# Performance work log

Measured on AMD Instinct MI355X. Metric: run time of the kernel, lower is better.

## Reference

```python
import jax, jax.numpy as jnp
import numpy as np

B, N, C = 4, 2048, 768
H = 12
DH = C // H
HID = int(C * 4.0)
SCALE = DH ** -0.5
EPS = 1e-5


def layernorm(x, g, b):
    mu = jnp.mean(x, axis=-1, keepdims=True)
    var = jnp.var(x, axis=-1, keepdims=True)
    return (x - mu) * jax.lax.rsqrt(var + EPS) * g + b


def setup_inputs() -> dict:
    key = jax.random.key(0)
    ks = jax.random.split(key, 10)
    s = lambda fan_in: 1.0 / np.sqrt(fan_in)
    return {
        "x": jax.random.normal(ks[0], (B, N, C), dtype=jnp.float32),
        "ln1_g": jnp.ones((C,), jnp.float32),
        "ln1_b": jnp.zeros((C,), jnp.float32),
        "w_qkv": jax.random.uniform(ks[1], (C, 3 * C), jnp.float32, -s(C), s(C)),
        "w_proj": jax.random.uniform(ks[2], (C, C), jnp.float32, -s(C), s(C)),
        "b_proj": jnp.zeros((C,), jnp.float32),
        "ln2_g": jnp.ones((C,), jnp.float32),
        "ln2_b": jnp.zeros((C,), jnp.float32),
        "w_fc1": jax.random.uniform(ks[3], (C, HID), jnp.float32, -s(C), s(C)),
        "b_fc1": jnp.zeros((HID,), jnp.float32),
        "w_fc2": jax.random.uniform(ks[4], (HID, C), jnp.float32, -s(HID), s(HID)),
        "b_fc2": jnp.zeros((C,), jnp.float32),
    }


def reference(x, ln1_g, ln1_b, w_qkv, w_proj, b_proj, ln2_g, ln2_b, w_fc1, b_fc1, w_fc2, b_fc2):
    # --- attention branch ---
    h = layernorm(x, ln1_g, ln1_b)                       # [B,N,C]
    qkv = (h @ w_qkv).reshape(B, N, 3, H, DH)
    q = qkv[:, :, 0].transpose(0, 2, 1, 3)               # [B,H,N,DH]
    k = qkv[:, :, 1].transpose(0, 2, 1, 3)
    v = qkv[:, :, 2].transpose(0, 2, 1, 3)
    attn = jnp.einsum('bhnd,bhmd->bhnm', q, k) * SCALE   # [B,H,N,N]
    attn = jax.nn.softmax(attn, axis=-1)
    y = jnp.einsum('bhnm,bhmd->bhnd', attn, v)           # [B,H,N,DH]
    y = y.transpose(0, 2, 1, 3).reshape(B, N, C)
    y = y @ w_proj + b_proj
    x = x + y
    # --- MLP branch ---
    h = layernorm(x, ln2_g, ln2_b)
    h = jax.nn.gelu(h @ w_fc1 + b_fc1, approximate=False)
    h = h @ w_fc2 + b_fc2
    return x + h
```

## Files before the change

kernel.cpp:

```cpp
#include <hip/hip_runtime.h>
#include <stdint.h>

#define DEV __device__ __forceinline__

typedef __attribute__((ext_vector_type(8))) short bf16x8;
typedef __attribute__((ext_vector_type(4))) float f32x4;
typedef __attribute__((ext_vector_type(4))) short s16x4;

DEV short f2bf(float f) {
    union { float f; unsigned u; } v; v.f = f;
    unsigned r = v.u + 0x7fffu + ((v.u >> 16) & 1u);
    return (short)(r >> 16);
}

DEV uint32_t cvtpk(float lo, float hi) {
    uint32_t r;
    asm("v_cvt_pk_bf16_f32 %0, %1, %2" : "=v"(r) : "v"(lo), "v"(hi));
    return r;
}

typedef const unsigned int __attribute__((address_space(1)))* gp1;
typedef unsigned int __attribute__((address_space(3)))* lp3;

DEV void gload16(const void* g, void* l) {
    __builtin_amdgcn_global_load_lds((gp1)g, (lp3)l, 16, 0, 0);
}

DEV void wait4_barrier() { asm volatile("s_waitcnt vmcnt(4)\ns_barrier" ::: "memory"); }
DEV void wait2_barrier() { asm volatile("s_waitcnt vmcnt(2)\ns_barrier" ::: "memory"); }
DEV void wait0_barrier() { asm volatile("s_waitcnt vmcnt(0)\ns_barrier" ::: "memory"); }

__global__ __launch_bounds__(256) void tcvt(
    const float* __restrict__ W, short* __restrict__ WT, int K, int N)
{
    __shared__ float t[32][33];
    int n0 = blockIdx.x * 32, k0 = blockIdx.y * 32;
    int tx = threadIdx.x & 31, ty = threadIdx.x >> 5;
#pragma unroll
    for (int i = 0; i < 32; i += 8)
        t[ty + i][tx] = W[(size_t)(k0 + ty + i) * N + n0 + tx];
    __syncthreads();
#pragma unroll
    for (int i = 0; i < 32; i += 8)
        WT[(size_t)(n0 + ty + i) * K + k0 + tx] = f2bf(t[tx][ty + i]);
}

__global__ __launch_bounds__(256) void ln_bf16(
    const float* __restrict__ x, const float* __restrict__ gam,
    const float* __restrict__ bet, short* __restrict__ out)
{
    const int w = threadIdx.x >> 6, lane = threadIdx.x & 63;
    const size_t row = (size_t)blockIdx.x * 4 + w;
    const float* xr = x + row * 768;
    float4 v[3];
    float s = 0.f, ss = 0.f;
#pragma unroll
    for (int k = 0; k < 3; ++k) {
        v[k] = *(const float4*)(xr + k * 256 + lane * 4);
        s  += v[k].x + v[k].y + v[k].z + v[k].w;
        ss += v[k].x * v[k].x + v[k].y * v[k].y + v[k].z * v[k].z + v[k].w * v[k].w;
    }
#pragma unroll
    for (int i = 1; i < 64; i <<= 1) { s += __shfl_xor(s, i, 64); ss += __shfl_xor(ss, i, 64); }
    const float inv = 1.f / 768.f;
    float mu = s * inv;
    float var = ss * inv - mu * mu;
    float rstd = rsqrtf(var + 1e-5f);
#pragma unroll
    for (int k = 0; k < 3; ++k) {
        int c = k * 256 + lane * 4;
        float vv[4] = { v[k].x, v[k].y, v[k].z, v[k].w };
        s16x4 o;
#pragma unroll
        for (int j = 0; j < 4; ++j)
            o[j] = f2bf((vv[j] - mu) * rstd * gam[c + j] + bet[c + j]);
        *(s16x4*)(out + row * 768 + c) = o;
    }
}

template<int MODE>
DEV void gemm_body(
    const short* __restrict__ A, const short* __restrict__ Bt,
    int M, int N, int K,
    const float* __restrict__ bias, const float* __restrict__ resid,
    float* __restrict__ outf, short* __restrict__ outb,
    short* __restrict__ qo, short* __restrict__ ko, short* __restrict__ vo,
    char* lds)
{
    const int tid = threadIdx.x;
    const int w = tid >> 6, lane = tid & 63;
    const int g = lane >> 4, l15 = lane & 15;
    const int brow = blockIdx.x * 128, bcol = blockIdx.y * 128;
    const int wr = w >> 2, wc = w & 3;
    f32x4 acc[4][2] = {};

    int aoff[4], boff[2];
#pragma unroll
    for (int m = 0; m < 4; ++m) {
        int ra = wr * 64 + m * 16 + l15;
        aoff[m] = ra * 64 + ((g * 16) ^ (((ra >> 1) & 3) << 4));
    }
#pragma unroll
    for (int n = 0; n < 2; ++n) {
        int rb = wc * 32 + n * 16 + l15;
        boff[n] = 8192 + rb * 64 + ((g * 16) ^ (((rb >> 1) & 3) << 4));
    }
    const int dStage = tid * 16;
    const char* pA; const char* pB;
    {
        int r = dStage >> 6, b = dStage & 63;
        int bs = b ^ (((r >> 1) & 3) << 4);
        pA = (const char*)(A  + (size_t)(brow + r) * K) + bs;
        pB = (const char*)(Bt + (size_t)(bcol + r) * K) + bs;
    }

#define GSTAGE(BUF, OFF) do { \
    gload16(pA + (OFF), lds + (BUF) * 16384 + dStage); \
    gload16(pB + (OFF), lds + (BUF) * 16384 + 8192 + dStage); } while (0)

    const int KT = K >> 5;
    GSTAGE(0, 0);
    GSTAGE(1, 64);
    wait2_barrier();

    const int NM = KT / 3;
    for (int mi = 0; mi < NM; ++mi) {
#pragma unroll
        for (int u = 0; u < 3; ++u) {
            const int s = mi * 3 + u;
            if (s + 2 < KT) GSTAGE((u + 2) % 3, (u + 2) * 64);
            bf16x8 af[4], bfg[2];
#pragma unroll
            for (int m = 0; m < 4; ++m)
                af[m]  = *(const bf16x8*)(lds + u * 16384 + aoff[m]);
#pragma unroll
            for (int n = 0; n < 2; ++n)
                bfg[n] = *(const bf16x8*)(lds + u * 16384 + boff[n]);
#pragma unroll
            for (int m = 0; m < 4; ++m)
#pragma unroll
                for (int n = 0; n < 2; ++n)
                    acc[m][n] = __builtin_amdgcn_mfma_f32_16x16x32_bf16(af[m], bfg[n], acc[m][n], 0, 0, 0);
            if (s + 1 < KT) {
                if (s + 2 < KT) wait2_barrier();
                else            wait0_barrier();
            }
        }
        pA += 192; pB += 192;
    }
#undef GSTAGE

#pragma unroll
    for (int m = 0; m < 4; ++m) {
#pragma unroll
        for (int n = 0; n < 2; ++n) {
#pragma unroll
            for (int j = 0; j < 4; ++j) {
                int r = brow + wr * 64 + m * 16 + g * 4 + j;
                int c = bcol + wc * 32 + n * 16 + l15;
                float v = acc[m][n][j];
                if (MODE == 0) {
                    int which = c / 768, cc = c % 768;
                    int h = cc >> 6, d = cc & 63;
                    int b_ = r >> 11, nn = r & 2047;
                    size_t bh = (size_t)b_ * 12 + h;
                    if (which == 0)      qo[(bh * 2048 + nn) * 64 + d] = f2bf(v * 0.18033688011112042f);
                    else if (which == 1) ko[(bh * 2048 + nn) * 64 + d] = f2bf(v);
                    else                 vo[(bh * 64 + d) * 2048 + nn] = f2bf(v);
                } else if (MODE == 1) {
                    outf[(size_t)r * N + c] = v + bias[c] + resid[(size_t)r * N + c];
                } else {
                    float t = v + bias[c];
                    float ge = 0.5f * t * (1.0f + erff(t * 0.70710678118654752f));
                    outb[(size_t)r * N + c] = f2bf(ge);
                }
            }
        }
    }
}

__global__ __launch_bounds__(512, 6) void g_qkv(
    const short* A, const short* Bt, int M, int N, int K,
    short* qo, short* ko, short* vo)
{
    __shared__ __align__(16) char lds[49152];
    gemm_body<0>(A, Bt, M, N, K, nullptr, nullptr, nullptr, nullptr, qo, ko, vo, lds);
}
__global__ __launch_bounds__(512, 6) void g_proj(
    const short* A, const short* Bt, int M, int N, int K,
    const float* bias, const float* resid, float* outf)
{
    __shared__ __align__(16) char lds[49152];
    gemm_body<1>(A, Bt, M, N, K, bias, resid, outf, nullptr, nullptr, nullptr, nullptr, lds);
}
__global__ __launch_bounds__(512, 6) void g_fc1(
    const short* A, const short* Bt, int M, int N, int K,
    const float* bias, short* outb)
{
    __shared__ __align__(16) char lds[49152];
    gemm_body<2>(A, Bt, M, N, K, bias, nullptr, nullptr, outb, nullptr, nullptr, nullptr, lds);
}
__global__ __launch_bounds__(512, 6) void g_fc2(
    const short* A, const short* Bt, int M, int N, int K,
    const float* bias, const float* resid, float* outf)
{
    __shared__ __align__(16) char lds[49152];
    gemm_body<1>(A, Bt, M, N, K, bias, resid, outf, nullptr, nullptr, nullptr, nullptr, lds);
}

__global__ __launch_bounds__(256, 3) void attn_fwd(
    const short* __restrict__ Q, const short* __restrict__ Kg,
    const short* __restrict__ Vt, short* __restrict__ Y)
{
    __shared__ __align__(16) char alds[40960];
    const int tid = threadIdx.x, w = tid >> 6, lane = tid & 63;
    const int g = lane >> 4, l15 = lane & 15;
    const int bh = blockIdx.y;
    const int q0 = blockIdx.x * 128 + w * 32;
    const short* Qb = Q  + (size_t)bh * 2048 * 64;
    const short* Kb = Kg + (size_t)bh * 2048 * 64;
    const short* Vb = Vt + (size_t)bh * 64 * 2048;

    bf16x8 qf[2][2];
#pragma unroll
    for (int m = 0; m < 2; ++m)
#pragma unroll
        for (int kk = 0; kk < 2; ++kk)
            qf[m][kk] = *(const bf16x8*)(Qb + (size_t)(q0 + m * 16 + l15) * 64 + kk * 32 + g * 8);

    f32x4 accO[2][4] = {};
    float lpart[2] = { 0.f, 0.f };

    int koff[2][2], voff[4], poff[2], pwoff[2][2];
#pragma unroll
    for (int n = 0; n < 2; ++n) {
        int key = n * 16 + l15;
#pragma unroll
        for (int kk = 0; kk < 2; ++kk)
            koff[kk][n] = key * 128 + ((kk * 64 + g * 16) ^ ((key & 7) << 4));
    }
#pragma unroll
    for (int n = 0; n < 4; ++n) {
        int d = n * 16 + l15;
        voff[n] = 16384 + d * 64 + ((g * 16) ^ (((d >> 1) & 3) << 4));
    }
#pragma unroll
    for (int m = 0; m < 2; ++m) {
        int qr = m * 16 + l15;
        int sw = ((qr >> 1) & 3) << 4;
        poff[m] = 32768 + w * 2048 + qr * 64 + ((g * 16) ^ sw);
#pragma unroll
        for (int n = 0; n < 2; ++n)
            pwoff[m][n] = 32768 + w * 2048 + qr * 64 + ((n * 32 + g * 8) ^ sw);
    }
    int dK, dV; const char* pK3; const char* pV3;
    {
        int bb = w * 1024;
        int L = bb + lane * 16;
        int rk = L >> 7, bk_ = L & 127;
        int bsk = bk_ ^ ((rk & 7) << 4);
        dK = bb;
        pK3 = (const char*)(Kb + (size_t)rk * 64) + bsk;
        int rv = L >> 6, bv = L & 63;
        int bsv = bv ^ (((rv >> 1) & 3) << 4);
        dV = bb;
        pV3 = (const char*)(Vb + (size_t)rv * 2048) + bsv;
    }
    gload16(pK3,        alds + dK);
    gload16(pV3,        alds + 16384 + dV);
    gload16(pK3 + 4096, alds + dK + 4096);
    gload16(pV3 + 64,   alds + 16384 + dV + 4096);
    gload16(pK3 + 8192, alds + dK + 8192);
    gload16(pV3 + 128,  alds + 16384 + dV + 8192);
    pK3 += 3 * 4096; pV3 += 3 * 64;
    wait4_barrier();

    for (int tm = 0; tm < 16; ++tm) {
#pragma unroll
        for (int tu = 0; tu < 4; ++tu) {
            const int t = tm * 4 + tu;
            if (t + 3 < 64) {
                gload16(pK3, alds + dK + ((tu + 3) & 3) * 4096);
                gload16(pV3, alds + 16384 + dV + ((tu + 3) & 3) * 4096);
                pK3 += 4096; pV3 += 64;
            }

            f32x4 s2[2][2] = {};
            __builtin_amdgcn_s_setprio(1);
#pragma unroll
            for (int kk = 0; kk < 2; ++kk) {
                bf16x8 kf[2];
#pragma unroll
                for (int n = 0; n < 2; ++n)
                    kf[n] = *(const bf16x8*)(alds + tu * 4096 + koff[kk][n]);
#pragma unroll
                for (int m = 0; m < 2; ++m)
#pragma unroll
                    for (int n = 0; n < 2; ++n)
                        s2[m][n] = __builtin_amdgcn_mfma_f32_16x16x32_bf16(kf[n], qf[m][kk], s2[m][n], 0, 0, 0);
            }
            __builtin_amdgcn_s_setprio(0);

#pragma unroll
            for (int m = 0; m < 2; ++m)
#pragma unroll
                for (int n = 0; n < 2; ++n) {
                    float e0 = __builtin_amdgcn_exp2f(s2[m][n][0]);
                    float e1 = __builtin_amdgcn_exp2f(s2[m][n][1]);
                    float e2 = __builtin_amdgcn_exp2f(s2[m][n][2]);
                    float e3 = __builtin_amdgcn_exp2f(s2[m][n][3]);
                    lpart[m] += (e0 + e1) + (e2 + e3);
                    uint2 pk; pk.x = cvtpk(e0, e1); pk.y = cvtpk(e2, e3);
                    *(uint2*)(alds + pwoff[m][n]) = pk;
                }

            __builtin_amdgcn_s_setprio(1);
            {
                bf16x8 vf[4], pf[2];
#pragma unroll
                for (int n = 0; n < 4; ++n)
                    vf[n] = *(const bf16x8*)(alds + tu * 4096 + voff[n]);
#pragma unroll
                for (int m = 0; m < 2; ++m)
                    pf[m] = *(const bf16x8*)(alds + poff[m]);
#pragma unroll
                for (int m = 0; m < 2; ++m)
#pragma unroll
                    for (int n = 0; n < 4; ++n)
                        accO[m][n] = __builtin_amdgcn_mfma_f32_16x16x32_bf16(pf[m], vf[n], accO[m][n], 0, 0, 0);
            }
            __builtin_amdgcn_s_setprio(0);

            if (t < 61)       wait4_barrier();
            else if (t == 61) wait2_barrier();
            else if (t == 62) wait0_barrier();
        }
    }

#pragma unroll
    for (int m = 0; m < 2; ++m) {
        lpart[m] += __shfl_xor(lpart[m], 16, 64);
        lpart[m] += __shfl_xor(lpart[m], 32, 64);
    }

    int b_ = bh / 12, h = bh % 12;
#pragma unroll
    for (int m = 0; m < 2; ++m) {
        float linv[4];
#pragma unroll
        for (int j = 0; j < 4; ++j)
            linv[j] = 1.0f / __shfl(lpart[m], g * 4 + j, 64);
#pragma unroll
        for (int n = 0; n < 4; ++n)
#pragma unroll
            for (int j = 0; j < 4; ++j) {
                int qq = q0 + m * 16 + g * 4 + j;
                int d = n * 16 + l15;
                Y[((size_t)b_ * 2048 + qq) * 768 + h * 64 + d] = f2bf(accO[m][n][j] * linv[j]);
            }
    }
}

extern "C" void kernel_launch(void* const* d_in, const int* in_sizes, int n_in,
                              void* d_out, int out_size, void* d_ws, size_t ws_size,
                              hipStream_t stream)
{
    const float* x      = (const float*)d_in[0];
    const float* ln1_g  = (const float*)d_in[1];
    const float* ln1_b  = (const float*)d_in[2];
    const float* w_qkv  = (const float*)d_in[3];
    const float* w_proj = (const float*)d_in[4];
    const float* b_proj = (const float*)d_in[5];
    const float* ln2_g  = (const float*)d_in[6];
    const float* ln2_b  = (const float*)d_in[7];
    const float* w_fc1  = (const float*)d_in[8];
    const float* b_fc1  = (const float*)d_in[9];
    const float* w_fc2  = (const float*)d_in[10];
    const float* b_fc2  = (const float*)d_in[11];

    char* ws = (char*)d_ws;
    size_t off = 0;
    auto alloc = [&](size_t bytes) -> void* {
        void* p = ws + off; off += (bytes + 255) & ~(size_t)255; return p;
    };
    short* wqkvT = (short*)alloc((size_t)2304 * 768 * 2);
    short* wprojT= (short*)alloc((size_t)768 * 768 * 2);
    short* wfc1T = (short*)alloc((size_t)3072 * 768 * 2);
    short* wfc2T = (short*)alloc((size_t)768 * 3072 * 2);
    short* h1    = (short*)alloc((size_t)8192 * 768 * 2);
    short* qb    = (short*)alloc((size_t)48 * 2048 * 64 * 2);
    short* kb    = (short*)alloc((size_t)48 * 2048 * 64 * 2);
    short* vtb   = (short*)alloc((size_t)48 * 64 * 2048 * 2);
    short* yb    = (short*)alloc((size_t)8192 * 768 * 2);
    float* X1    = (float*)alloc((size_t)8192 * 768 * 4);
    short* h2    = (short*)alloc((size_t)8192 * 768 * 2);
    short* h3    = (short*)alloc((size_t)8192 * 3072 * 2);

    tcvt<<<dim3(2304 / 32, 768 / 32),  256, 0, stream>>>(w_qkv,  wqkvT,  768,  2304);
    tcvt<<<dim3(768 / 32,  768 / 32),  256, 0, stream>>>(w_proj, wprojT, 768,  768);
    tcvt<<<dim3(3072 / 32, 768 / 32),  256, 0, stream>>>(w_fc1,  wfc1T,  768,  3072);
    tcvt<<<dim3(768 / 32,  3072 / 32), 256, 0, stream>>>(w_fc2,  wfc2T,  3072, 768);

    ln_bf16<<<2048, 256, 0, stream>>>(x, ln1_g, ln1_b, h1);

    g_qkv<<<dim3(64, 18), 512, 0, stream>>>(h1, wqkvT, 8192, 2304, 768, qb, kb, vtb);

    attn_fwd<<<dim3(16, 48), 256, 0, stream>>>(qb, kb, vtb, yb);

    g_proj<<<dim3(64, 6), 512, 0, stream>>>(yb, wprojT, 8192, 768, 768, b_proj, x, X1);

    ln_bf16<<<2048, 256, 0, stream>>>(X1, ln2_g, ln2_b, h2);

    g_fc1<<<dim3(64, 24), 512, 0, stream>>>(h2, wfc1T, 8192, 3072, 768, b_fc1, h3);

    g_fc2<<<dim3(64, 6), 512, 0, stream>>>(h3, wfc2T, 8192, 768, 3072, b_fc2, X1, (float*)d_out);
}
```

Measured before the change: 270.9 us.

## Use 256x128 block tiles for QKV and FC1 GEMMs

Adds a larger-tile GEMM variant (256x128 per block, 8 waves each computing 64x64) for the QKV and FC1 GEMMs. The goal is to raise arithmetic intensity and per-wave MFMA count relative to LDS reads and global loads. In exchange it uses 72KB of dynamic LDS and more accumulator registers, which lowers occupancy and halves the block count. The projection and FC2 GEMMs keep the original 128x128 kernel.

New measurement: 281.5 us. +3.9%, slower.

```diff
diff --git a/kernel.cpp b/kernel.cpp
--- a/kernel.cpp
+++ b/kernel.cpp
@@ -27,6 +27,7 @@
 }
 
 DEV void wait4_barrier() { asm volatile("s_waitcnt vmcnt(4)\ns_barrier" ::: "memory"); }
+DEV void wait3_barrier() { asm volatile("s_waitcnt vmcnt(3)\ns_barrier" ::: "memory"); }
 DEV void wait2_barrier() { asm volatile("s_waitcnt vmcnt(2)\ns_barrier" ::: "memory"); }
 DEV void wait0_barrier() { asm volatile("s_waitcnt vmcnt(0)\ns_barrier" ::: "memory"); }
 
@@ -79,49 +80,45 @@
 }
 
 template<int MODE>
-DEV void gemm_body(
+DEV void gemm_body_big(
     const short* __restrict__ A, const short* __restrict__ Bt,
     int M, int N, int K,
-    const float* __restrict__ bias, const float* __restrict__ resid,
-    float* __restrict__ outf, short* __restrict__ outb,
+    const float* __restrict__ bias, short* __restrict__ outb,
     short* __restrict__ qo, short* __restrict__ ko, short* __restrict__ vo,
     char* lds)
 {
     const int tid = threadIdx.x;
     const int w = tid >> 6, lane = tid & 63;
     const int g = lane >> 4, l15 = lane & 15;
-    const int brow = blockIdx.x * 128, bcol = blockIdx.y * 128;
-    const int wr = w >> 2, wc = w & 3;
-    f32x4 acc[4][2] = {};
-
-    int aoff[4], boff[2];
+    const int brow = blockIdx.x * 256, bcol = blockIdx.y * 128;
+    const int wr = w >> 1, wc = w & 1;
+    f32x4 acc[4][4] = {};
+
+    int aoff[4], boff[4];
 #pragma unroll
     for (int m = 0; m < 4; ++m) {
         int ra = wr * 64 + m * 16 + l15;
         aoff[m] = ra * 64 + ((g * 16) ^ (((ra >> 1) & 3) << 4));
-    }
-#pragma unroll
-    for (int n = 0; n < 2; ++n) {
-        int rb = wc * 32 + n * 16 + l15;
-        boff[n] = 8192 + rb * 64 + ((g * 16) ^ (((rb >> 1) & 3) << 4));
-    }
-    const int dStage = tid * 16;
-    const char* pA; const char* pB;
-    {
-        int r = dStage >> 6, b = dStage & 63;
-        int bs = b ^ (((r >> 1) & 3) << 4);
-        pA = (const char*)(A  + (size_t)(brow + r) * K) + bs;
-        pB = (const char*)(Bt + (size_t)(bcol + r) * K) + bs;
-    }
+        int rb = wc * 64 + m * 16 + l15;
+        boff[m] = 16384 + rb * 64 + ((g * 16) ^ (((rb >> 1) & 3) << 4));
+    }
+    const int L = tid * 16;
+    const int r0 = L >> 6, bb = L & 63;
+    const int bs = bb ^ (((r0 >> 1) & 3) << 4);
+    const char* pA0 = (const char*)(A  + (size_t)(brow + r0) * K) + bs;
+    const char* pA1 = (const char*)(A  + (size_t)(brow + 128 + r0) * K) + bs;
+    const char* pB  = (const char*)(Bt + (size_t)(bcol + r0) * K) + bs;
+    const int dA0 = L, dA1 = 8192 + L, dB = 16384 + L;
 
 #define GSTAGE(BUF, OFF) do { \
-    gload16(pA + (OFF), lds + (BUF) * 16384 + dStage); \
-    gload16(pB + (OFF), lds + (BUF) * 16384 + 8192 + dStage); } while (0)
+    gload16(pA0 + (OFF), lds + (BUF) * 24576 + dA0); \
+    gload16(pA1 + (OFF), lds + (BUF) * 24576 + dA1); \
+    gload16(pB  + (OFF), lds + (BUF) * 24576 + dB); } while (0)
 
     const int KT = K >> 5;
     GSTAGE(0, 0);
     GSTAGE(1, 64);
-    wait2_barrier();
+    wait3_barrier();
 
     const int NM = KT / 3;
     for (int mi = 0; mi < NM; ++mi) {
@@ -129,35 +126,34 @@
         for (int u = 0; u < 3; ++u) {
             const int s = mi * 3 + u;
             if (s + 2 < KT) GSTAGE((u + 2) % 3, (u + 2) * 64);
-            bf16x8 af[4], bfg[2];
+            bf16x8 af[4], bfg[4];
+#pragma unroll
+            for (int m = 0; m < 4; ++m) {
+                af[m]  = *(const bf16x8*)(lds + u * 24576 + aoff[m]);
+                bfg[m] = *(const bf16x8*)(lds + u * 24576 + boff[m]);
+            }
 #pragma unroll
             for (int m = 0; m < 4; ++m)
-                af[m]  = *(const bf16x8*)(lds + u * 16384 + aoff[m]);
-#pragma unroll
-            for (int n = 0; n < 2; ++n)
-                bfg[n] = *(const bf16x8*)(lds + u * 16384 + boff[n]);
-#pragma unroll
-            for (int m = 0; m < 4; ++m)
-#pragma unroll
-                for (int n = 0; n < 2; ++n)
+#pragma unroll
+                for (int n = 0; n < 4; ++n)
                     acc[m][n] = __builtin_amdgcn_mfma_f32_16x16x32_bf16(af[m], bfg[n], acc[m][n], 0, 0, 0);
             if (s + 1 < KT) {
-                if (s + 2 < KT) wait2_barrier();
+                if (s + 2 < KT) wait3_barrier();
                 else            wait0_barrier();
             }
         }
-        pA += 192; pB += 192;
+        pA0 += 192; pA1 += 192; pB += 192;
     }
 #undef GSTAGE
 
 #pragma unroll
     for (int m = 0; m < 4; ++m) {
 #pragma unroll
-        for (int n = 0; n < 2; ++n) {
+        for (int n = 0; n < 4; ++n) {
 #pragma unroll
             for (int j = 0; j < 4; ++j) {
                 int r = brow + wr * 64 + m * 16 + g * 4 + j;
-                int c = bcol + wc * 32 + n * 16 + l15;
+                int c = bcol + wc * 64 + n * 16 + l15;
                 float v = acc[m][n][j];
                 if (MODE == 0) {
                     int which = c / 768, cc = c % 768;
@@ -167,8 +163,6 @@
                     if (which == 0)      qo[(bh * 2048 + nn) * 64 + d] = f2bf(v * 0.18033688011112042f);
                     else if (which == 1) ko[(bh * 2048 + nn) * 64 + d] = f2bf(v);
                     else                 vo[(bh * 64 + d) * 2048 + nn] = f2bf(v);
-                } else if (MODE == 1) {
-                    outf[(size_t)r * N + c] = v + bias[c] + resid[(size_t)r * N + c];
                 } else {
                     float t = v + bias[c];
                     float ge = 0.5f * t * (1.0f + erff(t * 0.70710678118654752f));
@@ -179,33 +173,116 @@
     }
 }
 
-__global__ __launch_bounds__(512, 6) void g_qkv(
+__global__ __launch_bounds__(512, 4) void gb_qkv(
     const short* A, const short* Bt, int M, int N, int K,
     short* qo, short* ko, short* vo)
 {
-    __shared__ __align__(16) char lds[49152];
-    gemm_body<0>(A, Bt, M, N, K, nullptr, nullptr, nullptr, nullptr, qo, ko, vo, lds);
-}
+    extern __shared__ __align__(16) char lds[];
+    gemm_body_big<0>(A, Bt, M, N, K, nullptr, nullptr, qo, ko, vo, lds);
+}
+__global__ __launch_bounds__(512, 4) void gb_fc1(
+    const short* A, const short* Bt, int M, int N, int K,
+    const float* bias, short* outb)
+{
+    extern __shared__ __align__(16) char lds[];
+    gemm_body_big<2>(A, Bt, M, N, K, bias, outb, nullptr, nullptr, nullptr, lds);
+}
+
+template<int MODE>
+DEV void gemm_body(
+    const short* __restrict__ A, const short* __restrict__ Bt,
+    int M, int N, int K,
+    const float* __restrict__ bias, const float* __restrict__ resid,
+    float* __restrict__ outf, char* lds)
+{
+    const int tid = threadIdx.x;
+    const int w = tid >> 6, lane = tid & 63;
+    const int g = lane >> 4, l15 = lane & 15;
+    const int brow = blockIdx.x * 128, bcol = blockIdx.y * 128;
+    const int wr = w >> 2, wc = w & 3;
+    f32x4 acc[4][2] = {};
+
+    int aoff[4], boff[2];
+#pragma unroll
+    for (int m = 0; m < 4; ++m) {
+        int ra = wr * 64 + m * 16 + l15;
+        aoff[m] = ra * 64 + ((g * 16) ^ (((ra >> 1) & 3) << 4));
+    }
+#pragma unroll
+    for (int n = 0; n < 2; ++n) {
+        int rb = wc * 32 + n * 16 + l15;
+        boff[n] = 8192 + rb * 64 + ((g * 16) ^ (((rb >> 1) & 3) << 4));
+    }
+    const int dStage = tid * 16;
+    const char* pA; const char* pB;
+    {
+        int r = dStage >> 6, b = dStage & 63;
+        int bs = b ^ (((r >> 1) & 3) << 4);
+        pA = (const char*)(A  + (size_t)(brow + r) * K) + bs;
+        pB = (const char*)(Bt + (size_t)(bcol + r) * K) + bs;
+    }
+
+#define GSTAGE(BUF, OFF) do { \
+    gload16(pA + (OFF), lds + (BUF) * 16384 + dStage); \
+    gload16(pB + (OFF), lds + (BUF) * 16384 + 8192 + dStage); } while (0)
+
+    const int KT = K >> 5;
+    GSTAGE(0, 0);
+    GSTAGE(1, 64);
+    wait2_barrier();
+
+    const int NM = KT / 3;
+    for (int mi = 0; mi < NM; ++mi) {
+#pragma unroll
+        for (int u = 0; u < 3; ++u) {
+            const int s = mi * 3 + u;
+            if (s + 2 < KT) GSTAGE((u + 2) % 3, (u + 2) * 64);
+            bf16x8 af[4], bfg[2];
+#pragma unroll
+            for (int m = 0; m < 4; ++m)
+                af[m]  = *(const bf16x8*)(lds + u * 16384 + aoff[m]);
+#pragma unroll
+            for (int n = 0; n < 2; ++n)
+                bfg[n] = *(const bf16x8*)(lds + u * 16384 + boff[n]);
+#pragma unroll
+            for (int m = 0; m < 4; ++m)
+#pragma unroll
+                for (int n = 0; n < 2; ++n)
+                    acc[m][n] = __builtin_amdgcn_mfma_f32_16x16x32_bf16(af[m], bfg[n], acc[m][n], 0, 0, 0);
+            if (s + 1 < KT) {
+                if (s + 2 < KT) wait2_barrier();
+                else            wait0_barrier();
+            }
+        }
+        pA += 192; pB += 192;
+    }
+#undef GSTAGE
+
+#pragma unroll
+    for (int m = 0; m < 4; ++m)
+#pragma unroll
+        for (int n = 0; n < 2; ++n)
+#pragma unroll
+            for (int j = 0; j < 4; ++j) {
+                int r = brow + wr * 64 + m * 16 + g * 4 + j;
+                int c = bcol + wc * 32 + n * 16 + l15;
+                outf[(size_t)r * N + c] = acc[m][n][j] + bias[c] + resid[(size_t)r * N + c];
+            }
+}
+
 __global__ __launch_bounds__(512, 6) void g_proj(
     const short* A, const short* Bt, int M, int N, int K,
     const float* bias, const float* resid, float* outf)
 {
     __shared__ __align__(16) char lds[49152];
-    gemm_body<1>(A, Bt, M, N, K, bias, resid, outf, nullptr, nullptr, nullptr, nullptr, lds);
-}
-__global__ __launch_bounds__(512, 6) void g_fc1(
-    const short* A, const short* Bt, int M, int N, int K,
-    const float* bias, short* outb)
-{
-    __shared__ __align__(16) char lds[49152];
-    gemm_body<2>(A, Bt, M, N, K, bias, nullptr, nullptr, outb, nullptr, nullptr, nullptr, lds);
+    gemm_body<1>(A, Bt, M, N, K, bias, resid, outf, lds);
 }
 __global__ __launch_bounds__(512, 6) void g_fc2(
     const short* A, const short* Bt, int M, int N, int K,
     const float* bias, const float* resid, float* outf)
 {
     __shared__ __align__(16) char lds[49152];
-    gemm_body<1>(A, Bt, M, N, K, bias, resid, outf, nullptr, nullptr, nullptr, nullptr, lds);
+    gemm_body<1>(A, Bt, M, N, K, bias, resid, outf, lds);
 }
 
 __global__ __launch_bounds__(256, 3) void attn_fwd(
@@ -396,6 +473,9 @@
     short* h2    = (short*)alloc((size_t)8192 * 768 * 2);
     short* h3    = (short*)alloc((size_t)8192 * 3072 * 2);
 
+    hipFuncSetAttribute((const void*)gb_qkv, hipFuncAttributeMaxDynamicSharedMemorySize, 73728);
+    hipFuncSetAttribute((const void*)gb_fc1, hipFuncAttributeMaxDynamicSharedMemorySize, 73728);
+
     tcvt<<<dim3(2304 / 32, 768 / 32),  256, 0, stream>>>(w_qkv,  wqkvT,  768,  2304);
     tcvt<<<dim3(768 / 32,  768 / 32),  256, 0, stream>>>(w_proj, wprojT, 768,  768);
     tcvt<<<dim3(3072 / 32, 768 / 32),  256, 0, stream>>>(w_fc1,  wfc1T,  768,  3072);
@@ -403,7 +483,7 @@
 
     ln_bf16<<<2048, 256, 0, stream>>>(x, ln1_g, ln1_b, h1);
 
-    g_qkv<<<dim3(64, 18), 512, 0, stream>>>(h1, wqkvT, 8192, 2304, 768, qb, kb, vtb);
+    gb_qkv<<<dim3(32, 18), 512, 73728, stream>>>(h1, wqkvT, 8192, 2304, 768, qb, kb, vtb);
 
     attn_fwd<<<dim3(16, 48), 256, 0, stream>>>(qb, kb, vtb, yb);
 
@@ -411,7 +491,7 @@
 
     ln_bf16<<<2048, 256, 0, stream>>>(X1, ln2_g, ln2_b, h2);
 
-    g_fc1<<<dim3(64, 24), 512, 0, stream>>>(h2, wfc1T, 8192, 3072, 768, b_fc1, h3);
+    gb_fc1<<<dim3(32, 24), 512, 73728, stream>>>(h2, wfc1T, 8192, 3072, 768, b_fc1, h3);
 
     g_fc2<<<dim3(64, 6), 512, 0, stream>>>(h3, wfc2T, 8192, 768, 3072, b_fc2, X1, (float*)d_out);
 }
```
